# Kernel optimization log

Hardware: AMD Instinct MI355X
Metric: run time of the kernel (lower is better)

## Reference

```python
import jax, jax.numpy as jnp
import numpy as np

CLIP = 1e5  # state-update clip bound from the original code

def _H(x):
    # smooth heaviside: (tanh(1e7*x)+1)/2
    return (jnp.tanh(1e7 * x) + 1.0) * 0.5

def _interception(Prec, PET, INSC):
    insc = jnp.clip(INSC * 5.0, 0.5, 5.0)
    IMAX = jnp.maximum(jnp.minimum(insc, PET), 0.0)
    INT = jnp.maximum(jnp.minimum(IMAX, Prec), 0.0)
    INR = jnp.maximum(Prec - INT, 0.0)
    return INT, INR

def _sms_store(SMS1, SMSC):
    S = jnp.clip(SMSC * 500.0, 50.0, 500.0)
    return jnp.maximum(jnp.minimum(SMS1, S), 0.0)

def _soil_fluxes(PET, INT, INR, COEFF, SQ, SMSC, SUB, CRAK, SMS1):
    C = jnp.clip(COEFF * 400.0, 50.0, 400.0)
    q = jnp.clip(SQ * 6.0, 0.0, 6.0)
    S = jnp.clip(SMSC * 500.0, 50.0, 500.0)
    sub = jnp.clip(SUB, 0.0, 1.0)
    crak = jnp.clip(CRAK, 0.0, 1.0)
    infil = C * jnp.exp(-q * SMS1 / S)
    RMO = jnp.maximum(_H(infil - INR) * INR + _H(INR - infil) * infil, 0.0)
    IRUN = jnp.maximum(INR - RMO, 0.0)
    SRUN = jnp.maximum(sub * (SMS1 / S) * RMO, 0.0)
    REC = jnp.maximum(crak * (SMS1 / S) * (RMO - SRUN), 0.0)
    SMF = jnp.maximum(RMO - SRUN - REC, 0.0)
    POT = jnp.maximum(PET - INT, 0.0)
    cap = 10.0 * SMS1 / S
    ETS = jnp.maximum(_H(cap - POT) * POT + _H(POT - cap) * cap, 0.0)
    return RMO, IRUN, SRUN, REC, SMF, ETS

def _recharge(SMS1, SMSC, REC, SMF, ETS):
    S = jnp.clip(SMSC * 500.0, 50.0, 500.0)
    x = SMS1 + SMF - ETS - S
    return jnp.maximum(_H(x) * (REC + x) + _H(-x) * REC, 0.0)

def _gw_store(GW1, RecK, LG):
    lg = jnp.clip(LG * 0.1, 0.001, 0.1)
    rk = jnp.clip(RecK * 0.3, 0.003, 0.3)
    BAS = jnp.maximum(_H(GW1) * (rk * GW1), 0.0)
    GWL1 = GW1 - lg
    return BAS, GWL1

def _release(RS, SRUN, IRUN, BAS, RSmax, Area, Kr):
    kr = jnp.clip(Kr * 0.1, 0.01, 0.1)
    inflow = (IRUN + SRUN + BAS) * Area
    x = RS + inflow - RSmax
    Q_or = jnp.maximum(_H(x) * x, 0.0)
    Q_ir = jnp.maximum(_H(x) * (kr * RSmax) + _H(-x) * kr * RS * jnp.power(RS / RSmax, 1.5), 0.0)
    Q_res_in = jnp.maximum(inflow, 0.0)
    return Q_res_in, Q_or, Q_ir

def setup_inputs():
    key = jax.random.key(0)
    B, T = 4096, 2048
    u = jax.random.uniform(key, (B, T, 4), dtype=jnp.float32)
    Prec = u[..., 0:1] * 20.0          # precipitation (mm/day)
    PET = u[..., 1:2] * 5.0            # potential ET
    RSmax = u[..., 2:3] * 100.0 + 10.0 # reservoir capacity (>0 to avoid div-by-0)
    Area = u[..., 3:4] * 0.5           # area ratio in (0, 0.5)
    inputs = jnp.concatenate([Prec, PET, RSmax, Area], axis=-1)
    p = lambda: jnp.full((1,), 0.5, jnp.float32)
    return dict(inputs=inputs, INSC=p(), COEFF=p(), SQ=p(), SMSC=p(), SUB=p(),
                CRAK=p(), RecK=p(), Kr=p(), LG=p(), LS=p())

def reference(inputs, INSC, COEFF, SQ, SMSC, SUB, CRAK, RecK, Kr, LG, LS):
    B, T, _ = inputs.shape
    x_t = jnp.transpose(inputs, (1, 0, 2))  # [T,B,4]

    def step(state, x):
        SMS1, GW1, RS = state[:, 0:1], state[:, 1:2], state[:, 2:3]
        Prec, PET, RSmax, Area = x[:, 0:1], x[:, 1:2], x[:, 2:3], x[:, 3:4]
        INT, INR = _interception(Prec, PET, INSC)
        SMS1c = _sms_store(SMS1, SMSC)
        _, IRUN, SRUN, REC, SMF, ETS = _soil_fluxes(PET, INT, INR, COEFF, SQ, SMSC, SUB, CRAK, SMS1c)
        next_SMS = SMS1c + jnp.clip(SMF - ETS, -CLIP, CLIP)
        RECnew = _recharge(SMS1c, SMSC, REC, SMF, ETS)
        BAS, GWL1 = _gw_store(GW1, RecK, LG)
        next_GW = GWL1 + jnp.clip(RECnew - BAS, -CLIP, CLIP)
        Q_res_in, Q_or, Q_ir = _release(RS, SRUN, IRUN, BAS, RSmax, Area, Kr)
        next_RS = RS + jnp.clip(Q_res_in - Q_or - Q_ir, -CLIP, CLIP)
        new = jnp.concatenate([next_SMS, next_GW, next_RS], axis=1)
        return new, new

    init = jnp.zeros((B, 3), inputs.dtype)
    _, outs = jax.lax.scan(step, init, x_t)
    outs = jnp.transpose(outs, (1, 0, 2))  # [B,T,3]

    # shift stores by one step (as in original call(): tf.roll shift=1 axis=1)
    SMS1 = jnp.roll(outs[:, :, 0:1], 1, axis=1)
    GW1 = jnp.roll(outs[:, :, 1:2], 1, axis=1)
    RS = outs[:, :, 2:3]

    Prec, PET, RSmax, Area = inputs[..., 0:1], inputs[..., 1:2], inputs[..., 2:3], inputs[..., 3:4]
    INT, INR = _interception(Prec, PET, INSC)
    SMS1 = _sms_store(SMS1, SMSC)
    _, IRUN, SRUN, _, _, _ = _soil_fluxes(PET, INT, INR, COEFF, SQ, SMSC, SUB, CRAK, SMS1)
    BAS, _ = _gw_store(GW1, RecK, LG)
    _, Q_or, Q_ir = _release(RS, SRUN, IRUN, BAS, RSmax, Area, Kr)
    ls = jnp.clip(LS * 10.0, 0.01, 10.0)
    dr_arg = (SRUN + IRUN) * (1.0 - Area) + Q_ir + Q_or - ls
    DR = jnp.maximum(_H(dr_arg) * dr_arg, 0.0)
    GD = BAS * (1.0 - Area)
    Q = jnp.maximum(DR + GD, 0.0)  # [B,T,1] generated flow ('normal' mode)
    return Q
```

## Files before the change

### kernel.cpp

```cpp
#include <hip/hip_runtime.h>

#define T_LEN  2048
#define NCH    4096
#define CH     64
#define NCHUNK (T_LEN / CH)
#define WARM   256
#define TK     8
#define WPC    64

__device__ __forceinline__ float clampf(float x, float lo, float hi) {
    return fminf(fmaxf(x, lo), hi);
}

struct Params {
    float insc, C, S, sub, crak, rk, kr, lg, ls, invS, eca;
};

__device__ __forceinline__ Params mkparams(
    const float* pINSC, const float* pCOEFF, const float* pSQ, const float* pSMSC,
    const float* pSUB, const float* pCRAK, const float* pRecK, const float* pKr,
    const float* pLG, const float* pLS)
{
    Params pr;
    pr.insc = clampf(pINSC[0] * 5.f,   0.5f,   5.f);
    pr.C    = clampf(pCOEFF[0] * 400.f, 50.f,  400.f);
    float q = clampf(pSQ[0] * 6.f,     0.f,    6.f);
    pr.S    = clampf(pSMSC[0] * 500.f, 50.f,   500.f);
    pr.sub  = clampf(pSUB[0],          0.f,    1.f);
    pr.crak = clampf(pCRAK[0],         0.f,    1.f);
    pr.rk   = clampf(pRecK[0] * 0.3f,  0.003f, 0.3f);
    pr.kr   = clampf(pKr[0] * 0.1f,    0.01f,  0.1f);
    pr.lg   = clampf(pLG[0] * 0.1f,    0.001f, 0.1f);
    pr.ls   = clampf(pLS[0] * 10.f,    0.01f,  10.f);
    pr.invS = 1.0f / pr.S;
    pr.eca  = -q * pr.invS;
    return pr;
}

__device__ __forceinline__ void gload_lds16(const float4* g, float4* l) {
    __builtin_amdgcn_global_load_lds(
        (const __attribute__((address_space(1))) void*)(g),
        (__attribute__((address_space(3))) void*)(l),
        16, 0, 0);
}

template <bool OUT>
__device__ __forceinline__ float step_one(const Params& pr, const float4& xv,
                                          float& sms, float& gw, float& rs)
{
    const float p = xv.x, pet = xv.y, rsmax = xv.z, area = xv.w;

    const float INT  = fminf(fminf(pr.insc, pet), p);
    const float INR  = p - INT;
    const float smsc  = fminf(fmaxf(sms, 0.f), pr.S);
    const float ratio = smsc * pr.invS;
    const float infil = pr.C * __expf(pr.eca * smsc);
    const float RMO   = fminf(infil, INR);
    const float IRUN  = INR - RMO;
    const float SRUN  = pr.sub * ratio * RMO;
    const float REC   = pr.crak * ratio * (RMO - SRUN);
    const float SMF   = (RMO - SRUN) - REC;
    const float POT   = pet - INT;
    const float ETS   = fminf(POT, 10.f * ratio);
    const float nsms  = smsc + (SMF - ETS);
    const float RECn  = REC + fmaxf(nsms - pr.S, 0.f);
    const float BAS   = pr.rk * fmaxf(gw, 0.f);
    const float ngw   = (gw - pr.lg) + (RECn - BAS);
    const float inflow = (IRUN + SRUN + BAS) * area;
    const float rinv   = __builtin_amdgcn_rcpf(rsmax);
    const float xr     = (rs + inflow) - rsmax;
    const float Qor    = fmaxf(xr, 0.f);
    const float rrt    = rs * rinv;
    const float Qir    = (xr > 0.f) ? (pr.kr * rsmax)
                                    : (pr.kr * rs * (rrt * __builtin_amdgcn_sqrtf(rrt)));
    const float nrs    = rs + ((inflow - Qor) - Qir);

    float q = 0.f;
    if constexpr (OUT) {
        const float xq   = (nrs + inflow) - rsmax;
        const float Qor2 = fmaxf(xq, 0.f);
        const float r2   = nrs * rinv;
        const float Qir2 = (xq > 0.f) ? (pr.kr * rsmax)
                                      : (pr.kr * nrs * (r2 * __builtin_amdgcn_sqrtf(r2)));
        const float oma  = 1.f - area;
        const float dra  = (SRUN + IRUN) * oma + Qir2 + Qor2 - pr.ls;
        q = fmaxf(fmaxf(dra, 0.f) + BAS * oma, 0.f);
    }

    sms = nsms; gw = ngw; rs = nrs;
    return q;
}

__global__ __launch_bounds__(64)
void hirnn_chunk_kernel(const float* __restrict__ inp,
                        const float* __restrict__ pINSC, const float* __restrict__ pCOEFF,
                        const float* __restrict__ pSQ,   const float* __restrict__ pSMSC,
                        const float* __restrict__ pSUB,  const float* __restrict__ pCRAK,
                        const float* __restrict__ pRecK, const float* __restrict__ pKr,
                        const float* __restrict__ pLG,   const float* __restrict__ pLS,
                        float* __restrict__ out, float* __restrict__ ws)
{
    __shared__ float4 buf[2][WPC * TK];

    const int l     = threadIdx.x;
    const int blk   = blockIdx.x;
    const int chunk = blk >> 6;
    const int cgrp  = blk & 63;
    const int cbase = cgrp * WPC;
    const int chain = cbase + l;

    const Params pr = mkparams(pINSC, pCOEFF, pSQ, pSMSC, pSUB, pCRAK, pRecK, pKr, pLG, pLS);

    const int row  = l >> 3;
    const int scol = l & 7;
    const float4* __restrict__ gl =
        reinterpret_cast<const float4*>(inp) + (size_t)(cbase + row) * T_LEN + (scol ^ row);

    float4* __restrict__ qout = reinterpret_cast<float4*>(out + (size_t)chain * T_LEN);

    const int t_start = chunk * CH;
    const int t_warm  = (t_start >= WARM) ? (t_start - WARM) : 0;
    const int t_end   = t_start + CH;

    float sms = 0.f, gw = 0.f, rs = 0.f;

    auto issue_tile = [&](float4* dst, int t0) {
#pragma unroll
        for (int k = 0; k < TK; ++k)
            gload_lds16(gl + (size_t)(k * 8) * T_LEN + t0, dst + k * WPC);
    };

    issue_tile(&buf[0][0], t_warm);

    const int rbase = l * TK;
    const int rx    = l & 7;

    int p = 0;
    for (int t0 = t_warm; t0 < t_end; t0 += TK, p ^= 1) {
        if (t0 + TK < t_end) {
            issue_tile(&buf[p ^ 1][0], t0 + TK);
            asm volatile("s_waitcnt vmcnt(8)" ::: "memory");
        } else {
            asm volatile("s_waitcnt vmcnt(0)" ::: "memory");
        }
        __builtin_amdgcn_sched_barrier(0);

        const float4* bp = &buf[p][0];
        float4 x[TK];
#pragma unroll
        for (int s = 0; s < TK; ++s)
            x[s] = bp[rbase + (s ^ rx)];

        if (t0 < t_start) {
#pragma unroll
            for (int s = 0; s < TK; ++s) step_one<false>(pr, x[s], sms, gw, rs);
        } else {
            float q[TK];
#pragma unroll
            for (int s = 0; s < TK; ++s) q[s] = step_one<true>(pr, x[s], sms, gw, rs);
            float4 w0, w1;
            w0.x = q[0]; w0.y = q[1]; w0.z = q[2]; w0.w = q[3];
            w1.x = q[4]; w1.y = q[5]; w1.z = q[6]; w1.w = q[7];
            qout[t0 / 4 + 0] = w0;
            qout[t0 / 4 + 1] = w1;
        }
    }

    if (chunk == NCHUNK - 1) {
        ws[chain * 2 + 0] = sms;
        ws[chain * 2 + 1] = gw;
    }
}

__global__ __launch_bounds__(256)
void hirnn_t0_kernel(const float* __restrict__ inp,
                     const float* __restrict__ pINSC, const float* __restrict__ pCOEFF,
                     const float* __restrict__ pSQ,   const float* __restrict__ pSMSC,
                     const float* __restrict__ pSUB,  const float* __restrict__ pCRAK,
                     const float* __restrict__ pRecK, const float* __restrict__ pKr,
                     const float* __restrict__ pLG,   const float* __restrict__ pLS,
                     const float* __restrict__ ws, float* __restrict__ out)
{
    const int b = blockIdx.x * blockDim.x + threadIdx.x;
    if (b >= NCH) return;

    const Params pr = mkparams(pINSC, pCOEFF, pSQ, pSMSC, pSUB, pCRAK, pRecK, pKr, pLG, pLS);

    const float4 x0 = reinterpret_cast<const float4*>(inp)[(size_t)b * T_LEN];
    const float p = x0.x, pet = x0.y, rsmax = x0.z, area = x0.w;

    const float INT = fminf(fminf(pr.insc, pet), p);
    const float INR = p - INT;

    const float RMO0   = fminf(pr.C, INR);
    const float IRUN0  = INR - RMO0;
    const float infl0  = IRUN0 * area;
    const float xr0    = infl0 - rsmax;
    const float Qor0   = fmaxf(xr0, 0.f);
    const float Qir0   = (xr0 > 0.f) ? (pr.kr * rsmax) : 0.f;
    const float rs0    = infl0 - Qor0 - Qir0;

    const float smsF  = ws[b * 2 + 0];
    const float gwF   = ws[b * 2 + 1];
    const float smsc  = fminf(fmaxf(smsF, 0.f), pr.S);
    const float ratio = smsc * pr.invS;
    const float infil = pr.C * __expf(pr.eca * smsc);
    const float RMO   = fminf(infil, INR);
    const float IRUN  = INR - RMO;
    const float SRUN  = pr.sub * ratio * RMO;
    const float BAS   = pr.rk * fmaxf(gwF, 0.f);

    const float inflow = (IRUN + SRUN + BAS) * area;
    const float rinv   = __builtin_amdgcn_rcpf(rsmax);
    const float xq     = (rs0 + inflow) - rsmax;
    const float Qor2   = fmaxf(xq, 0.f);
    const float r2     = rs0 * rinv;
    const float Qir2   = (xq > 0.f) ? (pr.kr * rsmax)
                                    : (pr.kr * rs0 * (r2 * __builtin_amdgcn_sqrtf(r2)));
    const float oma    = 1.f - area;
    const float dra    = (SRUN + IRUN) * oma + Qir2 + Qor2 - pr.ls;
    out[(size_t)b * T_LEN] = fmaxf(fmaxf(dra, 0.f) + BAS * oma, 0.f);
}

extern "C" void kernel_launch(void* const* d_in, const int* in_sizes, int n_in,
                              void* d_out, int out_size, void* d_ws, size_t ws_size,
                              hipStream_t stream) {
    const float* inp = (const float*)d_in[0];
    float* out = (float*)d_out;
    float* ws  = (float*)d_ws;

    const int blocks = NCHUNK * (NCH / WPC);
    hirnn_chunk_kernel<<<blocks, WPC, 0, stream>>>(
        inp,
        (const float*)d_in[1], (const float*)d_in[2], (const float*)d_in[3],
        (const float*)d_in[4], (const float*)d_in[5], (const float*)d_in[6],
        (const float*)d_in[7], (const float*)d_in[8], (const float*)d_in[9],
        (const float*)d_in[10],
        out, ws);

    hirnn_t0_kernel<<<NCH / 256, 256, 0, stream>>>(
        inp,
        (const float*)d_in[1], (const float*)d_in[2], (const float*)d_in[3],
        (const float*)d_in[4], (const float*)d_in[5], (const float*)d_in[6],
        (const float*)d_in[7], (const float*)d_in[8], (const float*)d_in[9],
        (const float*)d_in[10],
        ws, out);
}
```

Before: 300.9 us.

## Deepen LDS prefetch pipeline to four buffers with smaller time tiles

Result: slower. 354.8 us (+17.9%).

```diff
diff --git a/kernel.cpp b/kernel.cpp
--- a/kernel.cpp
+++ b/kernel.cpp
@@ -5,7 +5,8 @@
 #define CH     64
 #define NCHUNK (T_LEN / CH)
 #define WARM   256
-#define TK     8
+#define TK     4
+#define NBUF   4
 #define WPC    64
 
 __device__ __forceinline__ float clampf(float x, float lo, float hi) {
@@ -100,21 +101,20 @@
                         const float* __restrict__ pLG,   const float* __restrict__ pLS,
                         float* __restrict__ out, float* __restrict__ ws)
 {
-    __shared__ float4 buf[2][WPC * TK];
+    __shared__ float4 buf[NBUF][WPC * TK];
 
     const int l     = threadIdx.x;
     const int blk   = blockIdx.x;
-    const int chunk = blk >> 6;
-    const int cgrp  = blk & 63;
+    const int chunk = blk & (NCHUNK - 1);
+    const int cgrp  = blk >> 5;
     const int cbase = cgrp * WPC;
     const int chain = cbase + l;
 
     const Params pr = mkparams(pINSC, pCOEFF, pSQ, pSMSC, pSUB, pCRAK, pRecK, pKr, pLG, pLS);
 
-    const int row  = l >> 3;
-    const int scol = l & 7;
     const float4* __restrict__ gl =
-        reinterpret_cast<const float4*>(inp) + (size_t)(cbase + row) * T_LEN + (scol ^ row);
+        reinterpret_cast<const float4*>(inp)
+        + (size_t)(cbase + (l >> 2)) * T_LEN + ((l & 3) ^ ((l >> 3) & 3));
 
     float4* __restrict__ qout = reinterpret_cast<float4*>(out + (size_t)chain * T_LEN);
 
@@ -127,21 +127,27 @@
     auto issue_tile = [&](float4* dst, int t0) {
 #pragma unroll
         for (int k = 0; k < TK; ++k)
-            gload_lds16(gl + (size_t)(k * 8) * T_LEN + t0, dst + k * WPC);
+            gload_lds16(gl + (size_t)(k * 16) * T_LEN + t0, dst + k * WPC);
     };
 
     issue_tile(&buf[0][0], t_warm);
+    issue_tile(&buf[1][0], t_warm + TK);
+    issue_tile(&buf[2][0], t_warm + 2 * TK);
 
     const int rbase = l * TK;
-    const int rx    = l & 7;
+    const int rx    = (l >> 1) & 3;
 
     int p = 0;
-    for (int t0 = t_warm; t0 < t_end; t0 += TK, p ^= 1) {
-        if (t0 + TK < t_end) {
-            issue_tile(&buf[p ^ 1][0], t0 + TK);
-            asm volatile("s_waitcnt vmcnt(8)" ::: "memory");
+    for (int t0 = t_warm; t0 < t_end; t0 += TK, p = (p + 1) & 3) {
+        const int t_pre = t0 + 3 * TK;
+        if (t_pre < t_end) {
+            issue_tile(&buf[(p + 3) & 3][0], t_pre);
+            asm volatile("s_waitcnt vmcnt(12)" ::: "memory");
         } else {
-            asm volatile("s_waitcnt vmcnt(0)" ::: "memory");
+            const int nrem = (t_end - t0) >> 2;
+            if (nrem == 3)      asm volatile("s_waitcnt vmcnt(8)" ::: "memory");
+            else if (nrem == 2) asm volatile("s_waitcnt vmcnt(4)" ::: "memory");
+            else                asm volatile("s_waitcnt vmcnt(0)" ::: "memory");
         }
         __builtin_amdgcn_sched_barrier(0);
 
@@ -158,11 +164,9 @@
             float q[TK];
 #pragma unroll
             for (int s = 0; s < TK; ++s) q[s] = step_one<true>(pr, x[s], sms, gw, rs);
-            float4 w0, w1;
-            w0.x = q[0]; w0.y = q[1]; w0.z = q[2]; w0.w = q[3];
-            w1.x = q[4]; w1.y = q[5]; w1.z = q[6]; w1.w = q[7];
-            qout[t0 / 4 + 0] = w0;
-            qout[t0 / 4 + 1] = w1;
+            float4 w;
+            w.x = q[0]; w.y = q[1]; w.z = q[2]; w.w = q[3];
+            qout[t0 / 4] = w;
         }
     }
 
```
